# Kernel optimization log

Hardware: AMD Instinct MI355X
Metric: run time of the kernel (lower is better)

## Reference

```python
import jax, jax.numpy as jnp
import numpy as np

N, L, C, S = 4096, 512, 16, 32


def setup_inputs() -> dict:
    key = jax.random.key(0)
    k1, k2, k3, k4 = jax.random.split(key, 4)
    raw = jax.random.normal(k1, (N, L, C), dtype=jnp.float32)
    # valid log-probs: logsumexp along C is slightly < 0
    log_input_probs = jax.nn.log_softmax(raw, axis=-1) - 0.01
    return {
        "log_input_probs": log_input_probs,
        "logit_initial_state_probs": jax.random.normal(k2, (S,), dtype=jnp.float32),
        "logit_transition_probs": jax.random.normal(k3, (S, C, S), dtype=jnp.float32),
        "logit_accepting_state_probs": jax.random.normal(k4, (S,), dtype=jnp.float32),
    }


def reference(log_input_probs, logit_initial_state_probs, logit_transition_probs,
              logit_accepting_state_probs):
    initial_state_probs = jax.nn.softmax(logit_initial_state_probs, axis=0)          # (S,)
    transition_probs = jax.nn.softmax(logit_transition_probs, axis=2)                # (S,C,S)
    accepting_log = jax.nn.log_sigmoid(logit_accepting_state_probs)                  # (S,)
    input_probs = jnp.exp(log_input_probs)                                           # (N,L,C)

    n = log_input_probs.shape[0]
    p0 = jnp.broadcast_to(initial_state_probs[None, :], (n, initial_state_probs.shape[0]))

    def step(p_state, x_t):
        # p_state: (N,S) prev-state probs; x_t: (N,C) symbol probs at step t
        p_new = jnp.einsum('bp,bc,pcn->bn', p_state, x_t, transition_probs)
        return p_new, None

    xs = jnp.swapaxes(input_probs, 0, 1)  # (L,N,C) for scan over time
    p_final, _ = jax.lax.scan(step, p0, xs)

    log_p_state = jnp.log(p_final + 1e-20)                                           # (N,S)
    log_acceptance = jax.nn.logsumexp(log_p_state + accepting_log[None, :], axis=1)  # (N,)
    return log_acceptance[None]  # (1,N)
```

## Files before the change

### kernel.cpp

```cpp
#include <hip/hip_runtime.h>
#include <math.h>

typedef _Float16 f16;
typedef _Float16 f16x2 __attribute__((ext_vector_type(2)));
typedef _Float16 f16x4 __attribute__((ext_vector_type(4)));
typedef _Float16 f16x8 __attribute__((ext_vector_type(8)));
typedef float    f32x4 __attribute__((ext_vector_type(4)));
typedef float    f32x16 __attribute__((ext_vector_type(16)));

#define NB 4096
#define LT 512
#define NC 16
#define NS 32

#define WS_P0     0
#define WS_SIG    128
#define WS_SUMSIG 256
#define WS_FWDT   512
#define WS_BWDT   (512 + 32768)
#define WS_F      (512 + 65536)
#define WS_G      (WS_F + 32*4096*4)

#if __has_builtin(__builtin_amdgcn_exp2f)
#define EXP2F __builtin_amdgcn_exp2f
#else
#define EXP2F exp2f
#endif

__global__ __launch_bounds__(512) void pdfa_prep(const float* __restrict__ tlogit,
                                                 const float* __restrict__ ilogit,
                                                 const float* __restrict__ alogit,
                                                 char* __restrict__ ws) {
    int tid = threadIdx.x;
    f16* fwdT = (f16*)(ws + WS_FWDT);
    f16* bwdT = (f16*)(ws + WS_BWDT);
    int p = tid >> 4, c = tid & 15;
    const float* row = tlogit + p * 512 + c * 32;
    float mx = row[0];
    for (int n = 1; n < 32; ++n) mx = fmaxf(mx, row[n]);
    float s = 0.f;
    for (int n = 0; n < 32; ++n) s += expf(row[n] - mx);
    float inv = 1.f / s;
    int ht = c >> 3, j = c & 7;
    for (int n = 0; n < 32; ++n) {
        float tv = expf(row[n] - mx) * inv;
        fwdT[p * 512 + (32 * ht + n) * 8 + j] = (f16)tv;
        bwdT[n * 512 + (32 * ht + p) * 8 + j] = (f16)tv;
    }
    if (tid < 32) {
        float m0 = ilogit[0];
        for (int n = 1; n < 32; ++n) m0 = fmaxf(m0, ilogit[n]);
        float s0 = 0.f;
        for (int n = 0; n < 32; ++n) s0 += expf(ilogit[n] - m0);
        ((float*)(ws + WS_P0))[tid]  = 256.f * expf(ilogit[tid] - m0) / s0;
        ((float*)(ws + WS_SIG))[tid] = 256.f / (1.f + expf(-alogit[tid]));
    }
    if (tid == 0) {
        float ss = 0.f;
        for (int n = 0; n < 32; ++n) ss += 1.f / (1.f + expf(-alogit[n]));
        *(float*)(ws + WS_SUMSIG) = ss;
    }
}

#define EC(v) ((f16)EXP2F((v) * 1.44269504089f))

#define XLOAD(A0,A1,T) { const f32x4* sp_ = (const f32x4*)(xbase + (size_t)(T) * NC); \
    A0 = sp_[0]; A1 = sp_[1]; }

#define XCONV(A0,A1) { \
    xq[0] = f16x2{EC(A0[0]), EC(A0[1])}; \
    xq[1] = f16x2{EC(A0[2]), EC(A0[3])}; \
    xq[2] = f16x2{EC(A1[0]), EC(A1[1])}; \
    xq[3] = f16x2{EC(A1[2]), EC(A1[3])}; }

#define KS(M, ACC, CIN) { \
    f16 pv_ = pnew[M]; \
    f16x2 pb_ = {pv_, pv_}; \
    f16x2 y0_ = pb_ * xq[0], y1_ = pb_ * xq[1], y2_ = pb_ * xq[2], y3_ = pb_ * xq[3]; \
    f16x8 bf_ = {y0_[0],y0_[1],y1_[0],y1_[1],y2_[0],y2_[1],y3_[0],y3_[1]}; \
    ACC = __builtin_amdgcn_mfma_f32_32x32x16_f16(af[M], bf_, CIN, 0, 0, 0); }

#define STEP(P, R0, R1, TNEXT) { \
    f32x16 a0_, a1_; \
    __builtin_amdgcn_s_setprio(1); \
    KS(0, a0_, z) KS(1, a1_, z) \
    KS(2, a0_, a0_) KS(3, a1_, a1_) \
    __builtin_amdgcn_s_setprio(0); \
    f32x16 pf_ = a0_ + a1_; \
    char* wb_ = lds_w + (P) * 18432; \
    *(f16x4*)(wb_ + 0  + 8*hi) = f16x4{(f16)pf_[0],  (f16)pf_[1],  (f16)pf_[2],  (f16)pf_[3]};  \
    *(f16x4*)(wb_ + 16 + 8*hi) = f16x4{(f16)pf_[4],  (f16)pf_[5],  (f16)pf_[6],  (f16)pf_[7]};  \
    *(f16x4*)(wb_ + 32 + 8*hi) = f16x4{(f16)pf_[8],  (f16)pf_[9],  (f16)pf_[10], (f16)pf_[11]}; \
    *(f16x4*)(wb_ + 48 + 8*hi) = f16x4{(f16)pf_[12], (f16)pf_[13], (f16)pf_[14], (f16)pf_[15]}; \
    __syncthreads(); \
    const char* rb_ = lds_r + (P) * 18432; \
    f16x4 q0_ = *(const f16x4*)(rb_); \
    f16x4 q1_ = *(const f16x4*)(rb_ + 1 * 2304); \
    f16x4 q2_ = *(const f16x4*)(rb_ + 2 * 2304); \
    f16x4 q3_ = *(const f16x4*)(rb_ + 3 * 2304); \
    f16x4 q4_ = *(const f16x4*)(rb_ + 4 * 2304); \
    f16x4 q5_ = *(const f16x4*)(rb_ + 5 * 2304); \
    f16x4 q6_ = *(const f16x4*)(rb_ + 6 * 2304); \
    f16x4 q7_ = *(const f16x4*)(rb_ + 7 * 2304); \
    XCONV(R0, R1) \
    XLOAD(R0, R1, TNEXT) \
    pnew = ((q0_ + q1_) + (q2_ + q3_)) + ((q4_ + q5_) + (q6_ + q7_)); }

__global__ __launch_bounds__(512, 1) void pdfa_main(const float* __restrict__ login,
                                                    char* __restrict__ ws) {
    __shared__ __align__(16) char partb[2][18432];
    const int tid  = threadIdx.x;
    const int w    = tid >> 6;
    const int lane = tid & 63;
    const int br   = tid & 31;
    const int hi   = (tid >> 5) & 1;
    const int bid  = blockIdx.x;
    const int dir  = bid & 1;
    const int b0   = (bid >> 1) << 5;

    const char* tblb = ws + (dir ? WS_BWDT : WS_FWDT);
    f16x8 af[4];
#pragma unroll
    for (int m = 0; m < 4; ++m)
        af[m] = *(const f16x8*)(tblb + (4 * w + m) * 1024 + lane * 16);

    const float* initv = (const float*)(ws + (dir ? WS_SIG : WS_P0));
    f16x4 pnew;
#pragma unroll
    for (int j = 0; j < 4; ++j) pnew[j] = (f16)initv[4 * w + j];

    const float* xbase = login + (size_t)(b0 + br) * (LT * NC) + 8 * hi;
    char* lds_w = &partb[0][0] + w * 2304 + br * 72;
    const char* lds_r = &partb[0][0] + br * 72 + 8 * w;
    const f32x16 z{};
    f16x2 xq[4];
    f32x4 xa0, xa1, xb0, xb1;

#define TT(S) (dir ? (511 - (S)) : (S))
    XLOAD(xa0, xa1, TT(0))
    XLOAD(xb0, xb1, TT(1))
    XCONV(xa0, xa1)
    XLOAD(xa0, xa1, TT(2))

    for (int s = 0; s < 256; s += 2) {
        STEP(0, xb0, xb1, TT(s + 3))
        STEP(1, xa0, xa1, TT(s + 4))
    }
#undef TT

    if (hi == 0) {
        float* outv = (float*)(ws + (dir ? WS_G : WS_F));
#pragma unroll
        for (int j = 0; j < 4; ++j)
            outv[(size_t)(4 * w + j) * NB + b0 + br] = (float)pnew[j];
    }
}

__global__ __launch_bounds__(256) void pdfa_combine(const char* __restrict__ ws,
                                                    float* __restrict__ out) {
    int b = blockIdx.x * 256 + threadIdx.x;
    const float* f = (const float*)(ws + WS_F);
    const float* g = (const float*)(ws + WS_G);
    float ss = *(const float*)(ws + WS_SUMSIG);
    float dot = 0.f;
#pragma unroll
    for (int s2 = 0; s2 < 32; ++s2)
        dot = fmaf(f[s2 * NB + b], g[s2 * NB + b], dot);
    out[b] = logf(dot * (1.f / 65536.f) + 1e-20f * ss);
}

extern "C" void kernel_launch(void* const* d_in, const int* in_sizes, int n_in,
                              void* d_out, int out_size, void* d_ws, size_t ws_size,
                              hipStream_t stream) {
    const float* login = (const float*)d_in[0];
    const float* ilog  = (const float*)d_in[1];
    const float* tlog  = (const float*)d_in[2];
    const float* alog  = (const float*)d_in[3];
    char* ws = (char*)d_ws;

    pdfa_prep<<<1, 512, 0, stream>>>(tlog, ilog, alog, ws);
    pdfa_main<<<256, 512, 0, stream>>>(login, ws);
    pdfa_combine<<<NB / 256, 256, 0, stream>>>(ws, (float*)d_out);
}
```

Before: 151.3 us.

## Share input-probability loads and exp conversion across waves via LDS

Before, every wave loaded all eight symbol log-probs per batch row and ran eight exponentials itself, so the same work was repeated across the 8 waves. Now each wave loads one scalar per row and time step, converts it to f16 and writes it to a double-buffered LDS slot. After the existing barrier each lane reads its f16x8 back, and the per-state scaling becomes a single f16x8 vector multiply. This cuts redundant global traffic and transcendental work, but it adds LDS writes and reads to the serial per-step critical path. It also issues narrow scalar global loads instead of vectorized ones.

```diff
diff --git a/kernel.cpp b/kernel.cpp
--- a/kernel.cpp
+++ b/kernel.cpp
@@ -64,36 +64,28 @@
 
 #define EC(v) ((f16)EXP2F((v) * 1.44269504089f))
 
-#define XLOAD(A0,A1,T) { const f32x4* sp_ = (const f32x4*)(xbase + (size_t)(T) * NC); \
-    A0 = sp_[0]; A1 = sp_[1]; }
-
-#define XCONV(A0,A1) { \
-    xq[0] = f16x2{EC(A0[0]), EC(A0[1])}; \
-    xq[1] = f16x2{EC(A0[2]), EC(A0[3])}; \
-    xq[2] = f16x2{EC(A1[0]), EC(A1[1])}; \
-    xq[3] = f16x2{EC(A1[2]), EC(A1[3])}; }
-
 #define KS(M, ACC, CIN) { \
     f16 pv_ = pnew[M]; \
-    f16x2 pb_ = {pv_, pv_}; \
-    f16x2 y0_ = pb_ * xq[0], y1_ = pb_ * xq[1], y2_ = pb_ * xq[2], y3_ = pb_ * xq[3]; \
-    f16x8 bf_ = {y0_[0],y0_[1],y1_[0],y1_[1],y2_[0],y2_[1],y3_[0],y3_[1]}; \
+    f16x8 pb_ = {pv_, pv_, pv_, pv_, pv_, pv_, pv_, pv_}; \
+    f16x8 bf_ = pb_ * xq8; \
     ACC = __builtin_amdgcn_mfma_f32_32x32x16_f16(af[M], bf_, CIN, 0, 0, 0); }
 
-#define STEP(P, R0, R1, TNEXT) { \
+#define STEP(P, XRAW, TNEXT) { \
     f32x16 a0_, a1_; \
     __builtin_amdgcn_s_setprio(1); \
     KS(0, a0_, z) KS(1, a1_, z) \
     KS(2, a0_, a0_) KS(3, a1_, a1_) \
     __builtin_amdgcn_s_setprio(0); \
     f32x16 pf_ = a0_ + a1_; \
-    char* wb_ = lds_w + (P) * 18432; \
+    char* wb_ = lds_pw + (P) * 18432; \
     *(f16x4*)(wb_ + 0  + 8*hi) = f16x4{(f16)pf_[0],  (f16)pf_[1],  (f16)pf_[2],  (f16)pf_[3]};  \
     *(f16x4*)(wb_ + 16 + 8*hi) = f16x4{(f16)pf_[4],  (f16)pf_[5],  (f16)pf_[6],  (f16)pf_[7]};  \
     *(f16x4*)(wb_ + 32 + 8*hi) = f16x4{(f16)pf_[8],  (f16)pf_[9],  (f16)pf_[10], (f16)pf_[11]}; \
     *(f16x4*)(wb_ + 48 + 8*hi) = f16x4{(f16)pf_[12], (f16)pf_[13], (f16)pf_[14], (f16)pf_[15]}; \
+    *(f16*)(lds_xw + (((P)^1) * 1280)) = EC(XRAW); \
+    XRAW = xg[(size_t)(TNEXT) * NC]; \
     __syncthreads(); \
-    const char* rb_ = lds_r + (P) * 18432; \
+    const char* rb_ = lds_pr + (P) * 18432; \
     f16x4 q0_ = *(const f16x4*)(rb_); \
     f16x4 q1_ = *(const f16x4*)(rb_ + 1 * 2304); \
     f16x4 q2_ = *(const f16x4*)(rb_ + 2 * 2304); \
@@ -102,13 +94,12 @@
     f16x4 q5_ = *(const f16x4*)(rb_ + 5 * 2304); \
     f16x4 q6_ = *(const f16x4*)(rb_ + 6 * 2304); \
     f16x4 q7_ = *(const f16x4*)(rb_ + 7 * 2304); \
-    XCONV(R0, R1) \
-    XLOAD(R0, R1, TNEXT) \
+    xq8 = *(const f16x8*)(lds_xr + (((P)^1) * 1280)); \
     pnew = ((q0_ + q1_) + (q2_ + q3_)) + ((q4_ + q5_) + (q6_ + q7_)); }
 
 __global__ __launch_bounds__(512, 1) void pdfa_main(const float* __restrict__ login,
                                                     char* __restrict__ ws) {
-    __shared__ __align__(16) char partb[2][18432];
+    __shared__ __align__(16) char partb[2 * 18432 + 2 * 1280];
     const int tid  = threadIdx.x;
     const int w    = tid >> 6;
     const int lane = tid & 63;
@@ -129,22 +120,29 @@
 #pragma unroll
     for (int j = 0; j < 4; ++j) pnew[j] = (f16)initv[4 * w + j];
 
-    const float* xbase = login + (size_t)(b0 + br) * (LT * NC) + 8 * hi;
-    char* lds_w = &partb[0][0] + w * 2304 + br * 72;
-    const char* lds_r = &partb[0][0] + br * 72 + 8 * w;
+    char* lds_pw = &partb[0] + w * 2304 + br * 72;
+    const char* lds_pr = &partb[0] + br * 72 + 8 * w;
+    char* xbase_lds = &partb[0] + 2 * 18432;
+    char* lds_xw = xbase_lds + br * 40 + (8 * hi + w) * 2;
+    const char* lds_xr = xbase_lds + br * 40 + hi * 16;
+
+    const float* xg = login + (size_t)(b0 + br) * (LT * NC) + 8 * hi + w;
+
     const f32x16 z{};
-    f16x2 xq[4];
-    f32x4 xa0, xa1, xb0, xb1;
+    f16x8 xq8;
+    float xrA, xrB;
 
 #define TT(S) (dir ? (511 - (S)) : (S))
-    XLOAD(xa0, xa1, TT(0))
-    XLOAD(xb0, xb1, TT(1))
-    XCONV(xa0, xa1)
-    XLOAD(xa0, xa1, TT(2))
+    xrA = xg[(size_t)TT(0) * NC];
+    xrB = xg[(size_t)TT(1) * NC];
+    *(f16*)(lds_xw) = EC(xrA);
+    xrA = xg[(size_t)TT(2) * NC];
+    __syncthreads();
+    xq8 = *(const f16x8*)(lds_xr);
 
     for (int s = 0; s < 256; s += 2) {
-        STEP(0, xb0, xb1, TT(s + 3))
-        STEP(1, xa0, xa1, TT(s + 4))
+        STEP(0, xrB, TT(s + 3))
+        STEP(1, xrA, TT(s + 4))
     }
 #undef TT
 
```

Measured after the change: 159.5 us. 5.4% more time.
